# Performance work log

Hardware: AMD Instinct MI355X
Metric: run time of the kernel (lower is better)

The kernel has to match this reference:

```python
import jax, jax.numpy as jnp
import numpy as np

WS = 8                 # window size (attn_grid_window_size)
N_WIN = WS * WS        # tokens per window = 64
EPS_LN = 1e-5

def _rel_index():
    # standard Swin/MaxViT relative position index for an 8x8 window
    coords = np.stack(np.meshgrid(np.arange(WS), np.arange(WS), indexing='ij')).reshape(2, -1)
    rel = coords[:, :, None] - coords[:, None, :]
    rel = rel.transpose(1, 2, 0).astype(np.int32)
    rel[..., 0] += WS - 1
    rel[..., 1] += WS - 1
    rel[..., 0] *= 2 * WS - 1
    return rel.sum(-1)  # [N_WIN, N_WIN] in [0, (2*WS-1)^2)

def layernorm(x, g, b):
    m = jnp.mean(x, -1, keepdims=True)
    v = jnp.mean((x - m) ** 2, -1, keepdims=True)
    return (x - m) * jax.lax.rsqrt(v + EPS_LN) * g + b

def l2norm(x):
    n = jnp.sqrt(jnp.sum(x * x, -1, keepdims=True))
    return x / jnp.maximum(n, 1e-12)  # torch F.normalize semantics

def setup_inputs() -> dict:
    key = jax.random.key(0)
    ks = jax.random.split(key, 4)
    B, C, H, W = 2, 256, 256, 256
    heads = 16
    s = 0.02
    return dict(
        X=jax.random.normal(ks[0], (B, C, H, W), jnp.float32),
        pre_g=jnp.ones((C,), jnp.float32), pre_b=jnp.zeros((C,), jnp.float32),
        post_g=jnp.ones((C,), jnp.float32), post_b=jnp.zeros((C,), jnp.float32),
        qkv_w=jax.random.normal(ks[1], (C, 3 * C), jnp.float32) * s,
        qkv_b=jnp.zeros((3 * C,), jnp.float32),
        proj_w=jax.random.normal(ks[2], (C, C), jnp.float32) * s,
        proj_b=jnp.zeros((C,), jnp.float32),
        rel_bias_table=jax.random.normal(ks[3], ((2 * WS - 1) ** 2, heads), jnp.float32) * s,
        rel_index=jnp.asarray(_rel_index()),
    )

def reference(X, pre_g, pre_b, post_g, post_b, qkv_w, qkv_b, proj_w, proj_b, rel_bias_table, rel_index):
    B, C, H, W = X.shape
    heads = rel_bias_table.shape[1]
    hd = C // heads
    # block partition: [B, C, H, W] -> [B*nH*nW, WS*WS, C]
    xw = X.reshape(B, C, H // WS, WS, W // WS, WS).transpose(0, 2, 4, 3, 5, 1)
    xw = xw.reshape(-1, N_WIN, C)
    Bw = xw.shape[0]
    # pre-norm + relative self-attention
    xn = layernorm(xw, pre_g, pre_b)
    qkv = (xn @ qkv_w + qkv_b).reshape(Bw, N_WIN, 3, heads, hd).transpose(2, 0, 3, 1, 4)
    q, k, v = qkv[0], qkv[1], qkv[2]            # [Bw, h, N, hd]
    q = l2norm(q)
    k = l2norm(k)                               # use_normalised_qk=True (MetNet-3)
    bias = rel_bias_table[rel_index.reshape(-1)].reshape(N_WIN, N_WIN, heads).transpose(2, 0, 1)
    attn = jax.nn.softmax(jnp.einsum('bhnd,bhmd->bhnm', q, k) + bias[None], axis=-1)
    out = jnp.einsum('bhnm,bhmd->bhnd', attn, v).transpose(0, 2, 1, 3).reshape(Bw, N_WIN, C)
    out = out @ proj_w + proj_b
    # residual, then post-norm branch (mlp = Identity)
    x = xw + out
    x = x + layernorm(x, post_g, post_b)
    # reverse partition -> [B, C, H, W]
    x = x.reshape(B, H // WS, W // WS, WS, WS, C).transpose(0, 5, 1, 3, 2, 4).reshape(B, C, H, W)
    return x
```

## Files before the change

### kernel.cpp

```cpp
#include <hip/hip_runtime.h>
#include <stdint.h>

typedef unsigned short u16;
typedef unsigned int   u32;

typedef short s8v __attribute__((ext_vector_type(8)));
typedef short s4v __attribute__((ext_vector_type(4)));
typedef float f4v __attribute__((ext_vector_type(4)));

struct __align__(8) US4 { u16 x, y, z, w; };
struct __align__(8) U2  { u32 a, b; };

__device__ __forceinline__ u16 f2bf(float f) {
    union { float f; u32 u; } v; v.f = f;
    u32 u = v.u;
    return (u16)((u + 0x7fffu + ((u >> 16) & 1u)) >> 16);
}

__device__ __forceinline__ u32 rbf(float x) { return __float_as_uint(x) + 0x8000u; }
__device__ __forceinline__ u32 pkbf(float lo, float hi) {
    return __builtin_amdgcn_perm(rbf(hi), rbf(lo), 0x07060302u);
}
__device__ __forceinline__ u32 pklo(u32 a, u32 b) {
    return __builtin_amdgcn_perm(b, a, 0x05040100u);
}
__device__ __forceinline__ u32 pkhi(u32 a, u32 b) {
    return __builtin_amdgcn_perm(b, a, 0x07060302u);
}

#define MFMA16(a, b, c) __builtin_amdgcn_mfma_f32_16x16x16bf16_1k((a), (b), (c), 0, 0, 0)
#define MFMA32(a, b, c) __builtin_amdgcn_mfma_f32_16x16x32_bf16((a), (b), (c), 0, 0, 0)

__global__ void pack_kernel(const float* __restrict__ qkv_w, const float* __restrict__ proj_w,
                            const float* __restrict__ table, const int* __restrict__ ridx,
                            u16* __restrict__ pkQ, u16* __restrict__ pkP, float* __restrict__ biasP)
{
    int tid = blockIdx.x * 256 + threadIdx.x;
    if (tid < 24576) {
        int g = tid;
        int lane = g & 63, ks = (g >> 6) & 7, mt = g >> 9;
        int quad = lane >> 4, c = lane & 15;
        union { u16 h[8]; s8v v; } tmp;
#pragma unroll
        for (int j = 0; j < 8; ++j) {
            int kk = ks * 32 + quad * 8 + j;
            tmp.h[j] = f2bf(qkv_w[kk * 768 + mt * 16 + c]);
        }
        *(s8v*)&pkQ[g * 8] = tmp.v;
    } else if (tid < 32768) {
        int g = tid - 24576;
        int lane = g & 63, ks = (g >> 6) & 7, mt = g >> 9;
        int quad = lane >> 4, c = lane & 15;
        union { u16 h[8]; s8v v; } tmp;
#pragma unroll
        for (int j = 0; j < 8; ++j) {
            int kk = ks * 32 + quad * 8 + j;
            tmp.h[j] = f2bf(proj_w[kk * 256 + mt * 16 + c]);
        }
        *(s8v*)&pkP[g * 8] = tmp.v;
    } else if (tid < 49152) {
        int g = tid - 32768;
        int h = g >> 10, rest = (g >> 6) & 15, lane = g & 63;
        int mt = rest >> 2, nt = rest & 3;
        int quad = lane >> 4, c = lane & 15;
        int query = nt * 16 + c;
#pragma unroll
        for (int r = 0; r < 4; ++r) {
            int key = mt * 16 + quad * 4 + r;
            biasP[g * 4 + r] = table[ridx[query * 64 + key] * 16 + h];
        }
    }
}

__global__ __launch_bounds__(512, 4)
void attn_win_kernel(const float* __restrict__ X,
                     const float* __restrict__ pre_g, const float* __restrict__ pre_b,
                     const float* __restrict__ post_g, const float* __restrict__ post_b,
                     const float* __restrict__ qkv_b, const float* __restrict__ proj_b,
                     const u16* __restrict__ pkQ, const u16* __restrict__ pkP,
                     const float* __restrict__ biasP,
                     float* __restrict__ out)
{
    __shared__ __align__(16) unsigned char smem[75264];
    u16*   xnS = (u16*)smem;
    u16*   vS  = (u16*)(smem + 33792);
    float* xf  = (float*)smem;
    float* pst = (float*)(smem + 70656);
    float* st  = (float*)(smem + 74752);

    const int tid  = threadIdx.x;
    const int w    = tid >> 6;
    const int l    = tid & 63;
    const int quad = l >> 4;
    const int cc   = l & 15;

    const int bidx = blockIdx.x;
    const int win  = ((bidx & 7) << 8) | (bidx >> 3);
    const int bb = win >> 10;
    const int wh = (win >> 5) & 31;
    const int ww = win & 31;
    const size_t base = (((size_t)bb * 256) * 256 + wh * 8) * 256 + ww * 8;

    const int ch0 = tid >> 4;
    const int t0  = (tid & 15) * 4;
    const int r0  = t0 >> 3, c0 = t0 & 7;

    f4v xv[8];
#pragma unroll
    for (int it = 0; it < 8; ++it) {
        int ch = it * 32 + ch0;
        xv[it] = *(const f4v*)(X + base + (size_t)ch * 65536 + r0 * 256 + c0);
    }

    {
        float s[4] = {0.f,0.f,0.f,0.f}, ss[4] = {0.f,0.f,0.f,0.f};
#pragma unroll
        for (int it = 0; it < 8; ++it)
#pragma unroll
            for (int j = 0; j < 4; ++j) { float x = xv[it][j]; s[j] += x; ss[j] += x * x; }
#pragma unroll
        for (int j = 0; j < 4; ++j) {
            s[j]  += __shfl_xor(s[j], 16, 64);  s[j]  += __shfl_xor(s[j], 32, 64);
            ss[j] += __shfl_xor(ss[j], 16, 64); ss[j] += __shfl_xor(ss[j], 32, 64);
        }
        if (quad == 0) {
#pragma unroll
            for (int j = 0; j < 4; ++j) {
                pst[(w * 64 + t0 + j) * 2]     = s[j];
                pst[(w * 64 + t0 + j) * 2 + 1] = ss[j];
            }
        }
    }
    __syncthreads();
    if (tid < 64) {
        float S = 0.f, SS = 0.f;
#pragma unroll
        for (int wv = 0; wv < 8; ++wv) {
            S  += pst[(wv * 64 + tid) * 2];
            SS += pst[(wv * 64 + tid) * 2 + 1];
        }
        float mean = S * (1.f / 256.f);
        float var  = SS * (1.f / 256.f) - mean * mean;
        st[tid * 2] = mean; st[tid * 2 + 1] = rsqrtf(var + 1e-5f);
    }
    __syncthreads();

    {
        float mean[4], rstd[4];
#pragma unroll
        for (int j = 0; j < 4; ++j) { mean[j] = st[(t0 + j) * 2]; rstd[j] = st[(t0 + j) * 2 + 1]; }
#pragma unroll
        for (int it = 0; it < 8; ++it) {
            int ch = it * 32 + ch0;
            float g = pre_g[ch], b = pre_b[ch];
            float y0 = (xv[it][0] - mean[0]) * rstd[0] * g + b;
            float y1 = (xv[it][1] - mean[1]) * rstd[1] * g + b;
            float y2 = (xv[it][2] - mean[2]) * rstd[2] * g + b;
            float y3 = (xv[it][3] - mean[3]) * rstd[3] * g + b;
            u32 m01 = pkbf(y0, y1);
            u32 m23 = pkbf(y2, y3);
            u32 p01 = __shfl_xor(m01, 16, 64);
            u32 p23 = __shfl_xor(m23, 16, 64);
            if ((quad & 1) == 0) {
                *(u32*)&xnS[(t0 + 0) * 264 + ch] = pklo(m01, p01);
                *(u32*)&xnS[(t0 + 1) * 264 + ch] = pkhi(m01, p01);
            } else {
                *(u32*)&xnS[(t0 + 2) * 264 + ch - 1] = pklo(p23, m23);
                *(u32*)&xnS[(t0 + 3) * 264 + ch - 1] = pkhi(p23, m23);
            }
        }
    }
    __syncthreads();

    u32 outbuf[2][4][2];
    const s8v* AQ = (const s8v*)pkQ;
#pragma unroll
    for (int hi = 0; hi < 2; ++hi) {
        const int head = w * 2 + hi;
        s4v qfr[4], kfr[4];
        {
            f4v acc0[4], acc1[4], acc2[4];
#pragma unroll
            for (int nt = 0; nt < 4; ++nt) { acc0[nt] = 0.f; acc1[nt] = 0.f; acc2[nt] = 0.f; }
#pragma unroll
            for (int ks = 0; ks < 8; ++ks) {
                s8v bfr[4];
#pragma unroll
                for (int nt = 0; nt < 4; ++nt)
                    bfr[nt] = *(const s8v*)&xnS[(nt * 16 + cc) * 264 + ks * 32 + quad * 8];
                s8v a0 = AQ[((head     ) * 8 + ks) * 64 + l];
                s8v a1 = AQ[((head + 16) * 8 + ks) * 64 + l];
                s8v a2 = AQ[((head + 32) * 8 + ks) * 64 + l];
#pragma unroll
                for (int nt = 0; nt < 4; ++nt) {
                    acc0[nt] = MFMA32(a0, bfr[nt], acc0[nt]);
                    acc1[nt] = MFMA32(a1, bfr[nt], acc1[nt]);
                    acc2[nt] = MFMA32(a2, bfr[nt], acc2[nt]);
                }
            }
            {
                float b0 = qkv_b[head * 16 + quad * 4 + 0];
                float b1 = qkv_b[head * 16 + quad * 4 + 1];
                float b2 = qkv_b[head * 16 + quad * 4 + 2];
                float b3 = qkv_b[head * 16 + quad * 4 + 3];
#pragma unroll
                for (int nt = 0; nt < 4; ++nt) {
                    f4v a = acc0[nt];
                    a[0] += b0; a[1] += b1; a[2] += b2; a[3] += b3;
                    float sq = (a[0]*a[0] + a[1]*a[1]) + (a[2]*a[2] + a[3]*a[3]);
                    sq += __shfl_xor(sq, 16, 64);
                    sq += __shfl_xor(sq, 32, 64);
                    float inv = 1.0f / fmaxf(sqrtf(sq), 1e-12f);
                    union { u32 d[2]; s4v v; } u;
                    u.d[0] = pkbf(a[0] * inv, a[1] * inv);
                    u.d[1] = pkbf(a[2] * inv, a[3] * inv);
                    qfr[nt] = u.v;
                }
            }
            {
                float b0 = qkv_b[(head + 16) * 16 + quad * 4 + 0];
                float b1 = qkv_b[(head + 16) * 16 + quad * 4 + 1];
                float b2 = qkv_b[(head + 16) * 16 + quad * 4 + 2];
                float b3 = qkv_b[(head + 16) * 16 + quad * 4 + 3];
#pragma unroll
                for (int nt = 0; nt < 4; ++nt) {
                    f4v a = acc1[nt];
                    a[0] += b0; a[1] += b1; a[2] += b2; a[3] += b3;
                    float sq = (a[0]*a[0] + a[1]*a[1]) + (a[2]*a[2] + a[3]*a[3]);
                    sq += __shfl_xor(sq, 16, 64);
                    sq += __shfl_xor(sq, 32, 64);
                    float inv = 1.0f / fmaxf(sqrtf(sq), 1e-12f);
                    union { u32 d[2]; s4v v; } u;
                    u.d[0] = pkbf(a[0] * inv, a[1] * inv);
                    u.d[1] = pkbf(a[2] * inv, a[3] * inv);
                    kfr[nt] = u.v;
                }
            }
            {
                float b0 = qkv_b[(head + 32) * 16 + quad * 4 + 0];
                float b1 = qkv_b[(head + 32) * 16 + quad * 4 + 1];
                float b2 = qkv_b[(head + 32) * 16 + quad * 4 + 2];
                float b3 = qkv_b[(head + 32) * 16 + quad * 4 + 3];
                int chb = head * 16 + quad * 4;
#pragma unroll
                for (int nt = 0; nt < 4; ++nt) {
                    f4v a = acc2[nt];
                    a[0] += b0; a[1] += b1; a[2] += b2; a[3] += b3;
                    int tok = nt * 16 + cc;
                    float p0 = __shfl_xor(a[0], 1, 64), p1 = __shfl_xor(a[1], 1, 64);
                    float p2 = __shfl_xor(a[2], 1, 64), p3 = __shfl_xor(a[3], 1, 64);
                    if ((l & 1) == 0) {
                        *(u32*)&vS[(chb + 0) * 72 + tok] = pkbf(a[0], p0);
                        *(u32*)&vS[(chb + 1) * 72 + tok] = pkbf(a[1], p1);
                    } else {
                        *(u32*)&vS[(chb + 2) * 72 + tok - 1] = pkbf(p2, a[2]);
                        *(u32*)&vS[(chb + 3) * 72 + tok - 1] = pkbf(p3, a[3]);
                    }
                }
            }
        }
        {
            s4v vfr[4];
#pragma unroll
            for (int kt = 0; kt < 4; ++kt)
                vfr[kt] = *(const s4v*)&vS[(head * 16 + cc) * 72 + kt * 16 + quad * 4];
            const f4v* BP = (const f4v*)biasP;
#pragma unroll
            for (int half = 0; half < 2; ++half) {
                f4v sT[4][2];
#pragma unroll
                for (int nt2 = 0; nt2 < 2; ++nt2) {
                    int nt = half * 2 + nt2;
#pragma unroll
                    for (int mt = 0; mt < 4; ++mt)
                        sT[mt][nt2] = MFMA16(kfr[mt], qfr[nt], BP[(head * 16 + mt * 4 + nt) * 64 + l]);
                }
#pragma unroll
                for (int nt2 = 0; nt2 < 2; ++nt2) {
                    int nt = half * 2 + nt2;
                    float m0 = fmaxf(fmaxf(sT[0][nt2][0], sT[0][nt2][1]), fmaxf(sT[0][nt2][2], sT[0][nt2][3]));
                    float m1 = fmaxf(fmaxf(sT[1][nt2][0], sT[1][nt2][1]), fmaxf(sT[1][nt2][2], sT[1][nt2][3]));
                    float m2 = fmaxf(fmaxf(sT[2][nt2][0], sT[2][nt2][1]), fmaxf(sT[2][nt2][2], sT[2][nt2][3]));
                    float m3 = fmaxf(fmaxf(sT[3][nt2][0], sT[3][nt2][1]), fmaxf(sT[3][nt2][2], sT[3][nt2][3]));
                    float mx = fmaxf(fmaxf(m0, m1), fmaxf(m2, m3));
                    mx = fmaxf(mx, __shfl_xor(mx, 16, 64));
                    mx = fmaxf(mx, __shfl_xor(mx, 32, 64));
                    float p[16];
                    float s4[4];
#pragma unroll
                    for (int mt = 0; mt < 4; ++mt) {
                        float e0 = __expf(sT[mt][nt2][0] - mx);
                        float e1 = __expf(sT[mt][nt2][1] - mx);
                        float e2 = __expf(sT[mt][nt2][2] - mx);
                        float e3 = __expf(sT[mt][nt2][3] - mx);
                        p[mt * 4 + 0] = e0; p[mt * 4 + 1] = e1;
                        p[mt * 4 + 2] = e2; p[mt * 4 + 3] = e3;
                        s4[mt] = (e0 + e1) + (e2 + e3);
                    }
                    float sum = (s4[0] + s4[1]) + (s4[2] + s4[3]);
                    sum += __shfl_xor(sum, 16, 64);
                    sum += __shfl_xor(sum, 32, 64);
                    float inv = 1.f / sum;
                    f4v o = 0.f;
#pragma unroll
                    for (int kt = 0; kt < 4; ++kt) {
                        union { u32 d[2]; s4v v; } up;
                        up.d[0] = pkbf(p[kt * 4 + 0], p[kt * 4 + 1]);
                        up.d[1] = pkbf(p[kt * 4 + 2], p[kt * 4 + 3]);
                        o = MFMA16(vfr[kt], up.v, o);
                    }
                    outbuf[hi][nt][0] = pkbf(o[0] * inv, o[1] * inv);
                    outbuf[hi][nt][1] = pkbf(o[2] * inv, o[3] * inv);
                }
            }
        }
    }
    __syncthreads();
#pragma unroll
    for (int hi = 0; hi < 2; ++hi)
#pragma unroll
        for (int nt = 0; nt < 4; ++nt) {
            U2 u2; u2.a = outbuf[hi][nt][0]; u2.b = outbuf[hi][nt][1];
            *(U2*)&xnS[(nt * 16 + cc) * 264 + (w * 2 + hi) * 16 + quad * 4] = u2;
        }
    __syncthreads();

    f4v xv2[8];
#pragma unroll
    for (int it = 0; it < 8; ++it) {
        int ch = it * 32 + ch0;
        xv2[it] = *(const f4v*)(X + base + (size_t)ch * 65536 + r0 * 256 + c0);
    }
    f4v pa0[4], pa1[4];
#pragma unroll
    for (int nt = 0; nt < 4; ++nt) { pa0[nt] = 0.f; pa1[nt] = 0.f; }
    {
        const s8v* AP = (const s8v*)pkP;
#pragma unroll
        for (int ks = 0; ks < 8; ++ks) {
            s8v bfr[4];
#pragma unroll
            for (int nt = 0; nt < 4; ++nt)
                bfr[nt] = *(const s8v*)&xnS[(nt * 16 + cc) * 264 + ks * 32 + quad * 8];
            s8v a0 = AP[((w * 2    ) * 8 + ks) * 64 + l];
            s8v a1 = AP[((w * 2 + 1) * 8 + ks) * 64 + l];
#pragma unroll
            for (int nt = 0; nt < 4; ++nt) {
                pa0[nt] = MFMA32(a0, bfr[nt], pa0[nt]);
                pa1[nt] = MFMA32(a1, bfr[nt], pa1[nt]);
            }
        }
    }
    __syncthreads();
    {
        int chb0 = (w * 2    ) * 16 + quad * 4;
        int chb1 = (w * 2 + 1) * 16 + quad * 4;
        float c00 = proj_b[chb0 + 0], c01 = proj_b[chb0 + 1], c02 = proj_b[chb0 + 2], c03 = proj_b[chb0 + 3];
        float c10 = proj_b[chb1 + 0], c11 = proj_b[chb1 + 1], c12 = proj_b[chb1 + 2], c13 = proj_b[chb1 + 3];
#pragma unroll
        for (int nt = 0; nt < 4; ++nt) {
            int tok = nt * 16 + cc;
            xf[(chb0 + 0) * 68 + tok] = pa0[nt][0] + c00;
            xf[(chb0 + 1) * 68 + tok] = pa0[nt][1] + c01;
            xf[(chb0 + 2) * 68 + tok] = pa0[nt][2] + c02;
            xf[(chb0 + 3) * 68 + tok] = pa0[nt][3] + c03;
            xf[(chb1 + 0) * 68 + tok] = pa1[nt][0] + c10;
            xf[(chb1 + 1) * 68 + tok] = pa1[nt][1] + c11;
            xf[(chb1 + 2) * 68 + tok] = pa1[nt][2] + c12;
            xf[(chb1 + 3) * 68 + tok] = pa1[nt][3] + c13;
        }
    }
    __syncthreads();

    f4v yv[8];
    {
        float s[4] = {0.f,0.f,0.f,0.f}, ss[4] = {0.f,0.f,0.f,0.f};
#pragma unroll
        for (int it = 0; it < 8; ++it) {
            int ch = it * 32 + ch0;
            f4v o = *(const f4v*)&xf[ch * 68 + t0];
            f4v y = xv2[it] + o;
            yv[it] = y;
#pragma unroll
            for (int j = 0; j < 4; ++j) { s[j] += y[j]; ss[j] += y[j] * y[j]; }
        }
#pragma unroll
        for (int j = 0; j < 4; ++j) {
            s[j]  += __shfl_xor(s[j], 16, 64);  s[j]  += __shfl_xor(s[j], 32, 64);
            ss[j] += __shfl_xor(ss[j], 16, 64); ss[j] += __shfl_xor(ss[j], 32, 64);
        }
        if (quad == 0) {
#pragma unroll
            for (int j = 0; j < 4; ++j) {
                pst[(w * 64 + t0 + j) * 2]     = s[j];
                pst[(w * 64 + t0 + j) * 2 + 1] = ss[j];
            }
        }
    }
    __syncthreads();
    if (tid < 64) {
        float S = 0.f, SS = 0.f;
#pragma unroll
        for (int wv = 0; wv < 8; ++wv) {
            S  += pst[(wv * 64 + tid) * 2];
            SS += pst[(wv * 64 + tid) * 2 + 1];
        }
        float mean = S * (1.f / 256.f);
        float var  = SS * (1.f / 256.f) - mean * mean;
        st[tid * 2] = mean; st[tid * 2 + 1] = rsqrtf(var + 1e-5f);
    }
    __syncthreads();

    {
        float mean[4], rstd[4];
#pragma unroll
        for (int j = 0; j < 4; ++j) { mean[j] = st[(t0 + j) * 2]; rstd[j] = st[(t0 + j) * 2 + 1]; }
#pragma unroll
        for (int it = 0; it < 8; ++it) {
            int ch = it * 32 + ch0;
            float g = post_g[ch], b = post_b[ch];
            f4v y = yv[it], z;
#pragma unroll
            for (int j = 0; j < 4; ++j)
                z[j] = y[j] + (y[j] - mean[j]) * rstd[j] * g + b;
            *(f4v*)(out + base + (size_t)ch * 65536 + r0 * 256 + c0) = z;
        }
    }
}

extern "C" void kernel_launch(void* const* d_in, const int* in_sizes, int n_in,
                              void* d_out, int out_size, void* d_ws, size_t ws_size,
                              hipStream_t stream)
{
    const float* X      = (const float*)d_in[0];
    const float* pre_g  = (const float*)d_in[1];
    const float* pre_b  = (const float*)d_in[2];
    const float* post_g = (const float*)d_in[3];
    const float* post_b = (const float*)d_in[4];
    const float* qkv_w  = (const float*)d_in[5];
    const float* qkv_b  = (const float*)d_in[6];
    const float* proj_w = (const float*)d_in[7];
    const float* proj_b = (const float*)d_in[8];
    const float* table  = (const float*)d_in[9];
    const int*   ridx   = (const int*)d_in[10];

    u16*   pkQ   = (u16*)d_ws;
    u16*   pkP   = (u16*)((char*)d_ws + 393216);
    float* biasP = (float*)((char*)d_ws + 524288);

    pack_kernel<<<192, 256, 0, stream>>>(qkv_w, proj_w, table, ridx, pkQ, pkP, biasP);
    attn_win_kernel<<<2048, 512, 0, stream>>>(X, pre_g, pre_b, post_g, post_b,
                                              qkv_b, proj_b, pkQ, pkP, biasP,
                                              (float*)d_out);
}
```

Baseline: 434.1 us.

## Keep V and projection outputs in registers to shrink LDS and raise occupancy

The V tile is no longer staged through shared memory; its MFMA fragments are rebuilt in registers with ds_bpermute and byte perms. The projection output goes straight into the residual and post-LayerNorm in MFMA fragment layout, which drops the xf scratch buffer and one barrier. X is now loaded and the output stored with scalar strided accesses that match the fragment layout. LDS falls from about 75KB to 38KB and the launch bound rises from 4 to 6 blocks, aiming at higher occupancy. In exchange, global memory access is less coalesced (scalar 4-byte accesses instead of float4), and register pressure rises under the tighter occupancy bound.

Measured after the change: 1.176 ms. 171% more time.

```diff
diff --git a/kernel.cpp b/kernel.cpp
--- a/kernel.cpp
+++ b/kernel.cpp
@@ -26,6 +26,9 @@
 }
 __device__ __forceinline__ u32 pkhi(u32 a, u32 b) {
     return __builtin_amdgcn_perm(b, a, 0x07060302u);
+}
+__device__ __forceinline__ u32 bperm(u32 byteaddr, u32 src) {
+    return (u32)__builtin_amdgcn_ds_bpermute((int)byteaddr, (int)src);
 }
 
 #define MFMA16(a, b, c) __builtin_amdgcn_mfma_f32_16x16x16bf16_1k((a), (b), (c), 0, 0, 0)
@@ -72,7 +75,7 @@
     }
 }
 
-__global__ __launch_bounds__(512, 4)
+__global__ __launch_bounds__(512, 6)
 void attn_win_kernel(const float* __restrict__ X,
                      const float* __restrict__ pre_g, const float* __restrict__ pre_b,
                      const float* __restrict__ post_g, const float* __restrict__ post_b,
@@ -81,12 +84,10 @@
                      const float* __restrict__ biasP,
                      float* __restrict__ out)
 {
-    __shared__ __align__(16) unsigned char smem[75264];
+    __shared__ __align__(16) unsigned char smem[38400];
     u16*   xnS = (u16*)smem;
-    u16*   vS  = (u16*)(smem + 33792);
-    float* xf  = (float*)smem;
-    float* pst = (float*)(smem + 70656);
-    float* st  = (float*)(smem + 74752);
+    float* pst = (float*)(smem + 33792);
+    float* st  = (float*)(smem + 37888);
 
     const int tid  = threadIdx.x;
     const int w    = tid >> 6;
@@ -178,6 +179,7 @@
     for (int hi = 0; hi < 2; ++hi) {
         const int head = w * 2 + hi;
         s4v qfr[4], kfr[4];
+        u32 vp01[4], vp23[4];
         {
             f4v acc0[4], acc1[4], acc2[4];
 #pragma unroll
@@ -241,29 +243,40 @@
                 float b1 = qkv_b[(head + 32) * 16 + quad * 4 + 1];
                 float b2 = qkv_b[(head + 32) * 16 + quad * 4 + 2];
                 float b3 = qkv_b[(head + 32) * 16 + quad * 4 + 3];
-                int chb = head * 16 + quad * 4;
 #pragma unroll
                 for (int nt = 0; nt < 4; ++nt) {
                     f4v a = acc2[nt];
-                    a[0] += b0; a[1] += b1; a[2] += b2; a[3] += b3;
-                    int tok = nt * 16 + cc;
-                    float p0 = __shfl_xor(a[0], 1, 64), p1 = __shfl_xor(a[1], 1, 64);
-                    float p2 = __shfl_xor(a[2], 1, 64), p3 = __shfl_xor(a[3], 1, 64);
-                    if ((l & 1) == 0) {
-                        *(u32*)&vS[(chb + 0) * 72 + tok] = pkbf(a[0], p0);
-                        *(u32*)&vS[(chb + 1) * 72 + tok] = pkbf(a[1], p1);
-                    } else {
-                        *(u32*)&vS[(chb + 2) * 72 + tok - 1] = pkbf(p2, a[2]);
-                        *(u32*)&vS[(chb + 3) * 72 + tok - 1] = pkbf(p3, a[3]);
-                    }
+                    vp01[nt] = pkbf(a[0] + b0, a[1] + b1);
+                    vp23[nt] = pkbf(a[2] + b2, a[3] + b3);
                 }
             }
         }
         {
             s4v vfr[4];
-#pragma unroll
-            for (int kt = 0; kt < 4; ++kt)
-                vfr[kt] = *(const s4v*)&vS[(head * 16 + cc) * 72 + kt * 16 + quad * 4];
+            {
+                u32 abase = (u32)((((cc >> 2) << 4) | (quad << 2)) << 2);
+                u32 psel  = (cc & 1) ? 0x07060302u : 0x05040100u;
+                bool useB = (cc & 2) != 0;
+#pragma unroll
+                for (int kt = 0; kt < 4; ++kt) {
+                    u32 ra0 = bperm(abase,      vp01[kt]);
+                    u32 ra1 = bperm(abase + 4,  vp01[kt]);
+                    u32 ra2 = bperm(abase + 8,  vp01[kt]);
+                    u32 ra3 = bperm(abase + 12, vp01[kt]);
+                    u32 rb0 = bperm(abase,      vp23[kt]);
+                    u32 rb1 = bperm(abase + 4,  vp23[kt]);
+                    u32 rb2 = bperm(abase + 8,  vp23[kt]);
+                    u32 rb3 = bperm(abase + 12, vp23[kt]);
+                    u32 s0 = useB ? rb0 : ra0;
+                    u32 s1 = useB ? rb1 : ra1;
+                    u32 s2 = useB ? rb2 : ra2;
+                    u32 s3 = useB ? rb3 : ra3;
+                    union { u32 d[2]; s4v v; } u;
+                    u.d[0] = __builtin_amdgcn_perm(s1, s0, psel);
+                    u.d[1] = __builtin_amdgcn_perm(s3, s2, psel);
+                    vfr[kt] = u.v;
+                }
+            }
             const f4v* BP = (const f4v*)biasP;
 #pragma unroll
             for (int half = 0; half < 2; ++half) {
@@ -325,11 +338,19 @@
         }
     __syncthreads();
 
-    f4v xv2[8];
-#pragma unroll
-    for (int it = 0; it < 8; ++it) {
-        int ch = it * 32 + ch0;
-        xv2[it] = *(const f4v*)(X + base + (size_t)ch * 65536 + r0 * 256 + c0);
+    const int chA = w * 32 + quad * 4;
+    const int chB = chA + 16;
+    const float* Xe = X + base + (cc & 7) + ((cc >> 3) << 8);
+    f4v xA[4], xB[4];
+#pragma unroll
+    for (int j = 0; j < 4; ++j) {
+        const float* pA = Xe + ((size_t)(chA + j) << 16);
+        const float* pB = Xe + ((size_t)(chB + j) << 16);
+#pragma unroll
+        for (int nt = 0; nt < 4; ++nt) {
+            xA[j][nt] = pA[nt << 9];
+            xB[j][nt] = pB[nt << 9];
+        }
     }
     f4v pa0[4], pa1[4];
 #pragma unroll
@@ -351,49 +372,39 @@
             }
         }
     }
-    __syncthreads();
+
+    f4v yA[4], yB[4];
+#pragma unroll
+    for (int j = 0; j < 4; ++j) {
+        float pbA = proj_b[chA + j], pbB = proj_b[chB + j];
+#pragma unroll
+        for (int nt = 0; nt < 4; ++nt) {
+            yA[j][nt] = xA[j][nt] + pa0[nt][j] + pbA;
+            yB[j][nt] = xB[j][nt] + pa1[nt][j] + pbB;
+        }
+    }
     {
-        int chb0 = (w * 2    ) * 16 + quad * 4;
-        int chb1 = (w * 2 + 1) * 16 + quad * 4;
-        float c00 = proj_b[chb0 + 0], c01 = proj_b[chb0 + 1], c02 = proj_b[chb0 + 2], c03 = proj_b[chb0 + 3];
-        float c10 = proj_b[chb1 + 0], c11 = proj_b[chb1 + 1], c12 = proj_b[chb1 + 2], c13 = proj_b[chb1 + 3];
-#pragma unroll
-        for (int nt = 0; nt < 4; ++nt) {
-            int tok = nt * 16 + cc;
-            xf[(chb0 + 0) * 68 + tok] = pa0[nt][0] + c00;
-            xf[(chb0 + 1) * 68 + tok] = pa0[nt][1] + c01;
-            xf[(chb0 + 2) * 68 + tok] = pa0[nt][2] + c02;
-            xf[(chb0 + 3) * 68 + tok] = pa0[nt][3] + c03;
-            xf[(chb1 + 0) * 68 + tok] = pa1[nt][0] + c10;
-            xf[(chb1 + 1) * 68 + tok] = pa1[nt][1] + c11;
-            xf[(chb1 + 2) * 68 + tok] = pa1[nt][2] + c12;
-            xf[(chb1 + 3) * 68 + tok] = pa1[nt][3] + c13;
-        }
-    }
-    __syncthreads();
-
-    f4v yv[8];
-    {
-        float s[4] = {0.f,0.f,0.f,0.f}, ss[4] = {0.f,0.f,0.f,0.f};
-#pragma unroll
-        for (int it = 0; it < 8; ++it) {
-            int ch = it * 32 + ch0;
-            f4v o = *(const f4v*)&xf[ch * 68 + t0];
-            f4v y = xv2[it] + o;
-            yv[it] = y;
-#pragma unroll
-            for (int j = 0; j < 4; ++j) { s[j] += y[j]; ss[j] += y[j] * y[j]; }
-        }
-#pragma unroll
-        for (int j = 0; j < 4; ++j) {
-            s[j]  += __shfl_xor(s[j], 16, 64);  s[j]  += __shfl_xor(s[j], 32, 64);
-            ss[j] += __shfl_xor(ss[j], 16, 64); ss[j] += __shfl_xor(ss[j], 32, 64);
+        float s[4], ss[4];
+#pragma unroll
+        for (int nt = 0; nt < 4; ++nt) {
+            float sv = 0.f, sq = 0.f;
+#pragma unroll
+            for (int j = 0; j < 4; ++j) {
+                float a = yA[j][nt], b = yB[j][nt];
+                sv += a + b; sq += a * a + b * b;
+            }
+            s[nt] = sv; ss[nt] = sq;
+        }
+#pragma unroll
+        for (int nt = 0; nt < 4; ++nt) {
+            s[nt]  += __shfl_xor(s[nt], 16, 64);  s[nt]  += __shfl_xor(s[nt], 32, 64);
+            ss[nt] += __shfl_xor(ss[nt], 16, 64); ss[nt] += __shfl_xor(ss[nt], 32, 64);
         }
         if (quad == 0) {
 #pragma unroll
-            for (int j = 0; j < 4; ++j) {
-                pst[(w * 64 + t0 + j) * 2]     = s[j];
-                pst[(w * 64 + t0 + j) * 2 + 1] = ss[j];
+            for (int nt = 0; nt < 4; ++nt) {
+                pst[(w * 64 + nt * 16 + cc) * 2]     = s[nt];
+                pst[(w * 64 + nt * 16 + cc) * 2 + 1] = ss[nt];
             }
         }
     }
@@ -410,20 +421,27 @@
         st[tid * 2] = mean; st[tid * 2 + 1] = rsqrtf(var + 1e-5f);
     }
     __syncthreads();
-
     {
         float mean[4], rstd[4];
 #pragma unroll
-        for (int j = 0; j < 4; ++j) { mean[j] = st[(t0 + j) * 2]; rstd[j] = st[(t0 + j) * 2 + 1]; }
-#pragma unroll
-        for (int it = 0; it < 8; ++it) {
-            int ch = it * 32 + ch0;
-            float g = post_g[ch], b = post_b[ch];
-            f4v y = yv[it], z;
-#pragma unroll
-            for (int j = 0; j < 4; ++j)
-                z[j] = y[j] + (y[j] - mean[j]) * rstd[j] * g + b;
-            *(f4v*)(out + base + (size_t)ch * 65536 + r0 * 256 + c0) = z;
+        for (int nt = 0; nt < 4; ++nt) {
+            mean[nt] = st[(nt * 16 + cc) * 2];
+            rstd[nt] = st[(nt * 16 + cc) * 2 + 1];
+        }
+        float* Oe = out + base + (cc & 7) + ((cc >> 3) << 8);
+#pragma unroll
+        for (int j = 0; j < 4; ++j) {
+            float gA = post_g[chA + j], bA = post_b[chA + j];
+            float gB = post_g[chB + j], bB = post_b[chB + j];
+            float* pA = Oe + ((size_t)(chA + j) << 16);
+            float* pB = Oe + ((size_t)(chB + j) << 16);
+#pragma unroll
+            for (int nt = 0; nt < 4; ++nt) {
+                float a = yA[j][nt];
+                float b = yB[j][nt];
+                pA[nt << 9] = a + (a - mean[nt]) * rstd[nt] * gA + bA;
+                pB[nt << 9] = b + (b - mean[nt]) * rstd[nt] * gB + bB;
+            }
         }
     }
 }
```
